# Kernel tuning notes

Measured on AMD Instinct MI355X. Metric: run time of the kernel, lower is better.

The kernel has to match this reference:

```python
import jax, jax.numpy as jnp
import numpy as np

# Quantization config (from Q_Act.set_bits / initialize usage)
N_LV = 16          # 4-bit inliers
QMAX = N_LV // 2 - 1   # 7
QMIN = -QMAX
N_LVA_O = 256      # 8-bit outliers
O_QMAX = N_LVA_O // 2 - 1  # 127
O_QMIN = -O_QMAX
N_REFRESH = 10


def setup_inputs() -> dict:
    key = jax.random.key(0)
    k1, k2 = jax.random.split(key)
    x = jax.random.normal(k1, (4, 4096, 2048), dtype=jnp.float32)
    # per-token scale, positive and well-conditioned
    s = jax.random.uniform(k2, (1, 4096, 1), dtype=jnp.float32) * 0.5 + 0.05
    return {"x": x, "s": s}


def _requant(x, s):
    # Faithful port of Q_Act.extracter_requant(x, 10, None, self.s, 'uni')
    B, L, D = x.shape
    R = N_REFRESH
    new_L = ((L + R - 1) // R) * R
    pad = new_L - L
    sf = s.reshape(L)
    if pad:
        x = jnp.concatenate([x, jnp.zeros((B, pad, D), x.dtype)], axis=1)
        sf = jnp.concatenate([sf, jnp.ones((pad,), sf.dtype)], axis=0)
    G = new_L // R
    xg = x.reshape(B, G, R, D).transpose(2, 0, 1, 3)   # [R, B, G, D]
    sg = sf.reshape(1, G, R).transpose(2, 0, 1)        # [R, 1, G]

    def step(o_list, inp):
        xi, si = inp                       # xi: [B,G,D], si: [1,G]
        inlier = xi * (1.0 - o_list)
        # dynamic scale check (global .any() branch, as in the torch code)
        dyn_s = jnp.max(jnp.abs(inlier), axis=-1) / QMAX   # [B,G]

        def upd(ol):
            a = jnp.abs(inlier)
            mean = jnp.mean(a, axis=-1, keepdims=True)
            std = jnp.std(a, axis=-1, ddof=1, keepdims=True)  # torch std is unbiased
            thr = mean + 3.0 * std
            return jnp.where((ol > 0) | (a > thr), 1.0, 0.0).astype(xi.dtype)

        o_new = jax.lax.cond(jnp.any(dyn_s > si), upd, lambda ol: ol, o_list)
        inlier2 = xi * (1.0 - o_new)
        sE = si[..., None]                                  # [1,G,1]
        # uniform quantization of inliers with static per-token scale
        in_x = jnp.clip(jnp.round(inlier2 / sE), QMIN, QMAX) * sE
        # 8-bit dynamic quantization of outliers (n_lva_o != 2**16 path)
        out_raw = xi * o_new
        out_s = jnp.clip(jnp.max(jnp.abs(out_raw), axis=-1, keepdims=True), 1e-8, None) / O_QMAX
        out_x = jnp.clip(jnp.round(out_raw / out_s), O_QMIN, O_QMAX) * out_s
        return o_new, in_x + out_x

    o0 = jnp.zeros((B, G, D), x.dtype)
    _, ys = jax.lax.scan(step, o0, (xg, sg))   # ys: [R, B, G, D]
    y = ys.transpose(1, 2, 0, 3).reshape(B, new_L, D)
    return y[:, :L, :]


def reference(x, s):
    # Q_Act.forward with n_lv != 0 and smoothing=True
    return _requant(x, s)
```

## Files before the change

### kernel.cpp

```cpp
#include <hip/hip_runtime.h>

#define L_TOK 4096
#define D_DIM 2048
#define R_STEPS 10
#define G_TOK 410
#define NROWS 1640
#define FB_NBLK 256

typedef unsigned int uint;
typedef unsigned long long u64;


__device__ __forceinline__ void load8(float* v, const float* p) {
  float4 a = *(const float4*)p;
  float4 b = *(const float4*)(p + 4);
  v[0] = a.x; v[1] = a.y; v[2] = a.z; v[3] = a.w;
  v[4] = b.x; v[5] = b.y; v[6] = b.z; v[7] = b.w;
}
__device__ __forceinline__ void zero8(float* v) {
#pragma unroll
  for (int i = 0; i < 8; ++i) v[i] = 0.0f;
}
__device__ __forceinline__ void store8(float* p, const float* v) {
  *(float4*)p = make_float4(v[0], v[1], v[2], v[3]);
  *(float4*)(p + 4) = make_float4(v[4], v[5], v[6], v[7]);
}

__global__ __launch_bounds__(256, 4) void qact_spec(
    const float* __restrict__ x, const float* __restrict__ s,
    float* __restrict__ y, uint* __restrict__ flagset) {
  __shared__ float redM[4];
  __shared__ double redS[4][2];
  __shared__ float redO[4];

  const int tid = threadIdx.x, lane = tid & 63, wid = tid >> 6;
  const int row = blockIdx.x;
  const int b = row / G_TOK, g = row % G_TOK;
  const size_t base = ((size_t)b * L_TOK + (size_t)g * R_STEPS) * D_DIM + (size_t)tid * 8;

  uint m = 0;
  float cur[8], nxt[8];
  load8(cur, x + base);

  for (int r = 0; r < R_STEPS; ++r) {
    const int tok = g * R_STEPS + r;
    const bool valid = tok < L_TOK;

    if (r + 1 < R_STEPS) {
      if (tok + 1 < L_TOK) load8(nxt, x + base + (size_t)(r + 1) * D_DIM);
      else zero8(nxt);
    }

    float a[8];
    float A = 0.0f;
    double S1 = 0.0, S2 = 0.0;
#pragma unroll
    for (int i = 0; i < 8; ++i) {
      a[i] = ((m >> i) & 1u) ? 0.0f : fabsf(cur[i]);
      A = fmaxf(A, a[i]);
      S1 += (double)a[i];
      S2 += (double)a[i] * (double)a[i];
    }
#pragma unroll
    for (int o = 32; o > 0; o >>= 1) {
      A = fmaxf(A, __shfl_down(A, o, 64));
      S1 += __shfl_down(S1, o, 64);
      S2 += __shfl_down(S2, o, 64);
    }
    if (lane == 0) { redM[wid] = A; redS[wid][0] = S1; redS[wid][1] = S2; }
    __syncthreads();
    A = fmaxf(fmaxf(redM[0], redM[1]), fmaxf(redM[2], redM[3]));
    S1 = redS[0][0] + redS[1][0] + redS[2][0] + redS[3][0];
    S2 = redS[0][1] + redS[1][1] + redS[2][1] + redS[3][1];

    const float sv = valid ? s[tok] : 1.0f;
    if (tid == 0) {
      if (A / 7.0f > sv) atomicOr(&flagset[r * 32], 1u);
    }

    const double n = (double)D_DIM;
    const double mean = S1 / n;
    double var = (S2 - n * mean * mean) / (n - 1.0);
    var = var > 0.0 ? var : 0.0;
    const double thr = mean + 3.0 * sqrt(var);
#pragma unroll
    for (int i = 0; i < 8; ++i)
      if ((double)a[i] > thr) m |= (1u << i);

    float O = 0.0f;
#pragma unroll
    for (int i = 0; i < 8; ++i)
      if ((m >> i) & 1u) O = fmaxf(O, fabsf(cur[i]));
#pragma unroll
    for (int o = 32; o > 0; o >>= 1) O = fmaxf(O, __shfl_down(O, o, 64));
    if (lane == 0) redO[wid] = O;
    __syncthreads();
    O = fmaxf(fmaxf(redO[0], redO[1]), fmaxf(redO[2], redO[3]));
    const float os = fmaxf(O, 1e-8f) / 127.0f;

    if (valid) {
      float out[8];
#pragma unroll
      for (int i = 0; i < 8; ++i) {
        const bool mm = (m >> i) & 1u;
        const float inl = mm ? 0.0f : cur[i];
        const float orr = mm ? cur[i] : 0.0f;
        const float qi = fminf(fmaxf(rintf(inl / sv), -7.0f), 7.0f);
        const float qo = fminf(fmaxf(rintf(orr / os), -127.0f), 127.0f);
        out[i] = qi * sv + qo * os;
      }
      store8(y + base + (size_t)r * D_DIM, out);
    }

#pragma unroll
    for (int i = 0; i < 8; ++i) cur[i] = nxt[i];
  }
}

__device__ __forceinline__ void grid_barrier(uint* cnt, uint* gen) {
  __syncthreads();
  if (threadIdx.x == 0) {
    const uint my = __hip_atomic_load(gen, __ATOMIC_ACQUIRE, __HIP_MEMORY_SCOPE_AGENT);
    const uint old = __hip_atomic_fetch_add(cnt, 1u, __ATOMIC_ACQ_REL, __HIP_MEMORY_SCOPE_AGENT);
    if (old == FB_NBLK - 1) {
      __hip_atomic_store(cnt, 0u, __ATOMIC_RELAXED, __HIP_MEMORY_SCOPE_AGENT);
      __hip_atomic_store(gen, my + 1u, __ATOMIC_RELEASE, __HIP_MEMORY_SCOPE_AGENT);
    } else {
      while (__hip_atomic_load(gen, __ATOMIC_ACQUIRE, __HIP_MEMORY_SCOPE_AGENT) == my)
        __builtin_amdgcn_s_sleep(8);
    }
  }
  __syncthreads();
}

__global__ __launch_bounds__(256, 2) void qact_fallback(
    const float* __restrict__ x, const float* __restrict__ s, float* __restrict__ y,
    const uint* __restrict__ flagset, uint* __restrict__ flags2, uint* __restrict__ bar) {
  bool ok = true;
#pragma unroll
  for (int r = 0; r < R_STEPS; ++r) ok &= (flagset[r * 32] != 0u);
  if (ok) return;

  __shared__ float redM[4];
  __shared__ double redS[4][2];
  __shared__ float redO[4];

  const int tid = threadIdx.x, lane = tid & 63, wid = tid >> 6;
  u64 mask = 0;

  for (int r = 0; r < R_STEPS; ++r) {
    for (int j = 0; j < 7; ++j) {
      const int row = blockIdx.x + FB_NBLK * j;
      if (row >= NROWS) break;
      const int b = row / G_TOK, g = row % G_TOK;
      const int tok = g * R_STEPS + r;
      float A = 0.0f;
      if (tok < L_TOK) {
        const size_t off = ((size_t)b * L_TOK + tok) * D_DIM + (size_t)tid * 8;
        float v[8];
        load8(v, x + off);
        const uint mj = (uint)(mask >> (j * 8)) & 0xffu;
#pragma unroll
        for (int i = 0; i < 8; ++i)
          if (!((mj >> i) & 1u)) A = fmaxf(A, fabsf(v[i]));
      }
#pragma unroll
      for (int o = 32; o > 0; o >>= 1) A = fmaxf(A, __shfl_down(A, o, 64));
      if (lane == 0) redM[wid] = A;
      __syncthreads();
      A = fmaxf(fmaxf(redM[0], redM[1]), fmaxf(redM[2], redM[3]));
      const float sv = (tok < L_TOK) ? s[tok] : 1.0f;
      if (tid == 0 && A / 7.0f > sv) atomicOr(&flags2[r * 32], 1u);
      __syncthreads();
    }

    grid_barrier(&bar[0], &bar[1]);

    const uint f = __hip_atomic_load(&flags2[r * 32], __ATOMIC_ACQUIRE, __HIP_MEMORY_SCOPE_AGENT);

    for (int j = 0; j < 7; ++j) {
      const int row = blockIdx.x + FB_NBLK * j;
      if (row >= NROWS) break;
      const int b = row / G_TOK, g = row % G_TOK;
      const int tok = g * R_STEPS + r;
      const bool valid = tok < L_TOK;
      const size_t off = ((size_t)b * L_TOK + (valid ? tok : 0)) * D_DIM + (size_t)tid * 8;
      float v[8];
      if (valid) load8(v, x + off);
      else zero8(v);
      uint mj = (uint)(mask >> (j * 8)) & 0xffu;
      float a[8];
#pragma unroll
      for (int i = 0; i < 8; ++i) a[i] = ((mj >> i) & 1u) ? 0.0f : fabsf(v[i]);
      if (f) {
        double S1 = 0.0, S2 = 0.0;
#pragma unroll
        for (int i = 0; i < 8; ++i) {
          S1 += (double)a[i];
          S2 += (double)a[i] * (double)a[i];
        }
#pragma unroll
        for (int o = 32; o > 0; o >>= 1) {
          S1 += __shfl_down(S1, o, 64);
          S2 += __shfl_down(S2, o, 64);
        }
        if (lane == 0) { redS[wid][0] = S1; redS[wid][1] = S2; }
        __syncthreads();
        S1 = redS[0][0] + redS[1][0] + redS[2][0] + redS[3][0];
        S2 = redS[0][1] + redS[1][1] + redS[2][1] + redS[3][1];
        const double n = (double)D_DIM;
        const double mean = S1 / n;
        double var = (S2 - n * mean * mean) / (n - 1.0);
        var = var > 0.0 ? var : 0.0;
        const double thr = mean + 3.0 * sqrt(var);
#pragma unroll
        for (int i = 0; i < 8; ++i)
          if ((double)a[i] > thr) mj |= (1u << i);
        mask = (mask & ~((u64)0xffu << (j * 8))) | ((u64)mj << (j * 8));
        __syncthreads();
      }
      if (valid) {
        float O = 0.0f;
#pragma unroll
        for (int i = 0; i < 8; ++i)
          if ((mj >> i) & 1u) O = fmaxf(O, fabsf(v[i]));
#pragma unroll
        for (int o = 32; o > 0; o >>= 1) O = fmaxf(O, __shfl_down(O, o, 64));
        if (lane == 0) redO[wid] = O;
        __syncthreads();
        O = fmaxf(fmaxf(redO[0], redO[1]), fmaxf(redO[2], redO[3]));
        const float os = fmaxf(O, 1e-8f) / 127.0f;
        const float sv = s[tok];
        float out[8];
#pragma unroll
        for (int i = 0; i < 8; ++i) {
          const bool mm = (mj >> i) & 1u;
          const float inl = mm ? 0.0f : v[i];
          const float orr = mm ? v[i] : 0.0f;
          const float qi = fminf(fmaxf(rintf(inl / sv), -7.0f), 7.0f);
          const float qo = fminf(fmaxf(rintf(orr / os), -127.0f), 127.0f);
          out[i] = qi * sv + qo * os;
        }
        store8(y + off, out);
        __syncthreads();
      }
    }
  }
}

extern "C" void kernel_launch(void* const* d_in, const int* in_sizes, int n_in,
                              void* d_out, int out_size, void* d_ws, size_t ws_size,
                              hipStream_t stream) {
  const float* x = (const float*)d_in[0];
  const float* s = (const float*)d_in[1];
  float* y = (float*)d_out;
  uint* flagset = (uint*)d_ws;
  uint* flags2 = (uint*)((char*)d_ws + 2048);
  uint* bar = (uint*)((char*)d_ws + 3968);

  hipMemsetAsync(d_ws, 0, 4096, stream);
  qact_spec<<<NROWS, 256, 0, stream>>>(x, s, y, flagset);
  qact_fallback<<<FB_NBLK, 256, 0, stream>>>(x, s, y, flagset, flags2, bar);
}
```

Baseline: 92.56 us.

## Fuse outlier-max reduction into main reduction and use nontemporal stores

The outlier max for the current step is now derived from the previous mask's max plus the unmasked max, compared against the new threshold. This removes the second block reduction and its barrier. Shared reduction buffers are double-buffered so one __syncthreads per step suffices. The change also simplifies the quantize arithmetic to a single divide per element, raises launch bounds occupancy to 8, and writes output with nontemporal stores. One risk is that the derived max is exact only when the newly flagged elements include the unmasked max element, which holds because the max exceeding the threshold implies it is flagged.

```diff
diff --git a/kernel.cpp b/kernel.cpp
--- a/kernel.cpp
+++ b/kernel.cpp
@@ -9,6 +9,7 @@
 
 typedef unsigned int uint;
 typedef unsigned long long u64;
+typedef float f32x4 __attribute__((ext_vector_type(4)));
 
 
 __device__ __forceinline__ void load8(float* v, const float* p) {
@@ -25,13 +26,18 @@
   *(float4*)p = make_float4(v[0], v[1], v[2], v[3]);
   *(float4*)(p + 4) = make_float4(v[4], v[5], v[6], v[7]);
 }
-
-__global__ __launch_bounds__(256, 4) void qact_spec(
+__device__ __forceinline__ void store8_nt(float* p, const float* v) {
+  f32x4 w0 = {v[0], v[1], v[2], v[3]};
+  f32x4 w1 = {v[4], v[5], v[6], v[7]};
+  __builtin_nontemporal_store(w0, (f32x4*)p);
+  __builtin_nontemporal_store(w1, (f32x4*)(p + 4));
+}
+
+__global__ __launch_bounds__(256, 8) void qact_spec(
     const float* __restrict__ x, const float* __restrict__ s,
     float* __restrict__ y, uint* __restrict__ flagset) {
-  __shared__ float redM[4];
-  __shared__ double redS[4][2];
-  __shared__ float redO[4];
+  __shared__ float redA[2][4], redB[2][4];
+  __shared__ double redS[2][4][2];
 
   const int tid = threadIdx.x, lane = tid & 63, wid = tid >> 6;
   const int row = blockIdx.x;
@@ -45,6 +51,8 @@
   for (int r = 0; r < R_STEPS; ++r) {
     const int tok = g * R_STEPS + r;
     const bool valid = tok < L_TOK;
+    const int buf = r & 1;
+    const float sv = valid ? s[tok] : 1.0f;
 
     if (r + 1 < R_STEPS) {
       if (tok + 1 < L_TOK) load8(nxt, x + base + (size_t)(r + 1) * D_DIM);
@@ -52,28 +60,36 @@
     }
 
     float a[8];
-    float A = 0.0f;
+    float A = 0.0f, Bm = 0.0f;
     double S1 = 0.0, S2 = 0.0;
 #pragma unroll
     for (int i = 0; i < 8; ++i) {
-      a[i] = ((m >> i) & 1u) ? 0.0f : fabsf(cur[i]);
+      const bool bit = (m >> i) & 1u;
+      const float fa = fabsf(cur[i]);
+      a[i] = bit ? 0.0f : fa;
       A = fmaxf(A, a[i]);
-      S1 += (double)a[i];
-      S2 += (double)a[i] * (double)a[i];
+      Bm = bit ? fmaxf(Bm, fa) : Bm;
+      const double ad = (double)a[i];
+      S1 += ad;
+      S2 += ad * ad;
     }
 #pragma unroll
     for (int o = 32; o > 0; o >>= 1) {
       A = fmaxf(A, __shfl_down(A, o, 64));
+      Bm = fmaxf(Bm, __shfl_down(Bm, o, 64));
       S1 += __shfl_down(S1, o, 64);
       S2 += __shfl_down(S2, o, 64);
     }
-    if (lane == 0) { redM[wid] = A; redS[wid][0] = S1; redS[wid][1] = S2; }
+    if (lane == 0) {
+      redA[buf][wid] = A; redB[buf][wid] = Bm;
+      redS[buf][wid][0] = S1; redS[buf][wid][1] = S2;
+    }
     __syncthreads();
-    A = fmaxf(fmaxf(redM[0], redM[1]), fmaxf(redM[2], redM[3]));
-    S1 = redS[0][0] + redS[1][0] + redS[2][0] + redS[3][0];
-    S2 = redS[0][1] + redS[1][1] + redS[2][1] + redS[3][1];
-
-    const float sv = valid ? s[tok] : 1.0f;
+    A = fmaxf(fmaxf(redA[buf][0], redA[buf][1]), fmaxf(redA[buf][2], redA[buf][3]));
+    Bm = fmaxf(fmaxf(redB[buf][0], redB[buf][1]), fmaxf(redB[buf][2], redB[buf][3]));
+    S1 = redS[buf][0][0] + redS[buf][1][0] + redS[buf][2][0] + redS[buf][3][0];
+    S2 = redS[buf][0][1] + redS[buf][1][1] + redS[buf][2][1] + redS[buf][3][1];
+
     if (tid == 0) {
       if (A / 7.0f > sv) atomicOr(&flagset[r * 32], 1u);
     }
@@ -87,15 +103,7 @@
     for (int i = 0; i < 8; ++i)
       if ((double)a[i] > thr) m |= (1u << i);
 
-    float O = 0.0f;
-#pragma unroll
-    for (int i = 0; i < 8; ++i)
-      if ((m >> i) & 1u) O = fmaxf(O, fabsf(cur[i]));
-#pragma unroll
-    for (int o = 32; o > 0; o >>= 1) O = fmaxf(O, __shfl_down(O, o, 64));
-    if (lane == 0) redO[wid] = O;
-    __syncthreads();
-    O = fmaxf(fmaxf(redO[0], redO[1]), fmaxf(redO[2], redO[3]));
+    const float O = ((double)A > thr) ? fmaxf(Bm, A) : Bm;
     const float os = fmaxf(O, 1e-8f) / 127.0f;
 
     if (valid) {
@@ -103,13 +111,13 @@
 #pragma unroll
       for (int i = 0; i < 8; ++i) {
         const bool mm = (m >> i) & 1u;
-        const float inl = mm ? 0.0f : cur[i];
-        const float orr = mm ? cur[i] : 0.0f;
-        const float qi = fminf(fmaxf(rintf(inl / sv), -7.0f), 7.0f);
-        const float qo = fminf(fmaxf(rintf(orr / os), -127.0f), 127.0f);
-        out[i] = qi * sv + qo * os;
-      }
-      store8(y + base + (size_t)r * D_DIM, out);
+        const float d = mm ? os : sv;
+        const float bound = mm ? 127.0f : 7.0f;
+        float q = rintf(cur[i] / d);
+        q = fminf(fmaxf(q, -bound), bound);
+        out[i] = q * d;
+      }
+      store8_nt(y + base + (size_t)r * D_DIM, out);
     }
 
 #pragma unroll
@@ -258,7 +266,7 @@
   uint* flags2 = (uint*)((char*)d_ws + 2048);
   uint* bar = (uint*)((char*)d_ws + 3968);
 
-  hipMemsetAsync(d_ws, 0, 4096, stream);
+  (void)hipMemsetAsync(d_ws, 0, 4096, stream);
   qact_spec<<<NROWS, 256, 0, stream>>>(x, s, y, flagset);
   qact_fallback<<<FB_NBLK, 256, 0, stream>>>(x, s, y, flagset, flags2, bar);
 }
```

New measurement: 100.0 us. 1.08x slower.
